# Kernel tuning notes

Measured on AMD Instinct MI355X. Metric: run time of the kernel, lower is better.

The kernel has to match this reference:

```python
import jax, jax.numpy as jnp
import numpy as np

N = 512
K = 32


def _laplacian_coo(n):
    """5-point stencil Laplacian on an n x n grid, COO (row, col, val)."""
    idx = np.arange(n * n).reshape(n, n)
    rows = [idx.ravel()]
    cols = [idx.ravel()]
    vals = [np.full(n * n, 4.0, dtype=np.float32)]
    # horizontal neighbors
    r = idx[:, 1:].ravel(); c = idx[:, :-1].ravel()
    rows += [r, c]; cols += [c, r]
    vals += [np.full(r.size, -1.0, dtype=np.float32)] * 2
    # vertical neighbors
    r = idx[1:, :].ravel(); c = idx[:-1, :].ravel()
    rows += [r, c]; cols += [c, r]
    vals += [np.full(r.size, -1.0, dtype=np.float32)] * 2
    return (np.concatenate(rows).astype(np.int32),
            np.concatenate(cols).astype(np.int32),
            np.concatenate(vals))


def setup_inputs() -> dict:
    key = jax.random.key(0)
    k_w, k_z = jax.random.split(key)
    # probe tensor with zeroed boundary (as in forward)
    w = jax.random.normal(k_w, (K, 1, N + 2, N + 2), dtype=jnp.float32)
    w = w.at[:, :, 0, :].set(0.0)
    w = w.at[:, :, -1, :].set(0.0)
    w = w.at[:, :, :, 0].set(0.0)
    w = w.at[:, :, :, -1].set(0.0)
    # stand-in for model(w): the network output flattened to (K, N*N)
    z = jax.random.normal(k_z, (K, N * N), dtype=jnp.float32)
    row, col, vals = _laplacian_coo(N)
    return {
        "w": w,
        "z": z,
        "row": jnp.asarray(row),
        "col": jnp.asarray(col),
        "vals": jnp.asarray(vals),
    }


def reference(w, z, row, col, vals):
    n2 = z.shape[1]                      # N*N
    # SpMM: Az = (A @ z^T)^T, done via gather + segment-sum over rows.
    gathered = vals[:, None] * z[:, col].T          # [nnz, K]
    Az = jax.ops.segment_sum(gathered, row, num_segments=n2).T  # [K, N*N]
    n = w.shape[-1] - 2
    w_interior = w[:, 0, 1:-1, 1:-1].reshape(w.shape[0], n * n)
    diff = w_interior - Az
    loss = jnp.mean(jnp.sum(diff * diff, axis=1))
    return loss
```

## Files before the change

### kernel.cpp

```cpp
#include <hip/hip_runtime.h>
#include <hip/hip_bf16.h>


#define N_GRID 512
#define K_PROBE 32
#define NN (N_GRID * N_GRID)
#define WROW (N_GRID + 2)
#define R_BAND 8
#define BANDS (N_GRID / R_BAND)
#define NBLOCKS ((K_PROBE * BANDS) / 2)

__global__ __launch_bounds__(256) void condition_loss_main(
    const float* __restrict__ w, const float* __restrict__ z,
    float* __restrict__ partial) {
    const int work = (blockIdx.x & 7) * (NBLOCKS / 8) + (blockIdx.x >> 3);

    const int band_g = work * 2 + (threadIdx.x >> 7);
    const int k    = band_g >> 6;
    const int band = band_g & 63;
    const int cg   = threadIdx.x & 127;
    const int col  = cg << 2;
    const int r0   = band * R_BAND;

    const float* __restrict__ zk = z + (long)k * NN + col;
    const float* __restrict__ wk =
        w + (long)k * (WROW * WROW) + (long)(r0 + 1) * WROW + (col + 1);

    float4 zm = make_float4(0.f, 0.f, 0.f, 0.f);
    if (r0 > 0) zm = *reinterpret_cast<const float4*>(zk + (long)(r0 - 1) * N_GRID);
    float4 zc = *reinterpret_cast<const float4*>(zk + (long)r0 * N_GRID);

    float acc = 0.0f;
#pragma unroll
    for (int r = 0; r < R_BAND; ++r) {
        const int i = r0 + r;
        float4 zp = make_float4(0.f, 0.f, 0.f, 0.f);
        if (i + 1 < N_GRID)
            zp = *reinterpret_cast<const float4*>(zk + (long)(i + 1) * N_GRID);
        const float zl = (col > 0)            ? zk[(long)i * N_GRID - 1] : 0.0f;
        const float zr = (col + 4 < N_GRID)   ? zk[(long)i * N_GRID + 4] : 0.0f;

        const float az0 = 4.0f * zc.x - zm.x - zp.x - zl   - zc.y;
        const float az1 = 4.0f * zc.y - zm.y - zp.y - zc.x - zc.z;
        const float az2 = 4.0f * zc.z - zm.z - zp.z - zc.y - zc.w;
        const float az3 = 4.0f * zc.w - zm.w - zp.w - zc.z - zr;

        const float* __restrict__ wr = wk + (long)r * WROW;
        const float d0 = wr[0] - az0;
        const float d1 = wr[1] - az1;
        const float d2 = wr[2] - az2;
        const float d3 = wr[3] - az3;
        acc += d0 * d0 + d1 * d1 + d2 * d2 + d3 * d3;

        zm = zc;
        zc = zp;
    }

    for (int off = 32; off > 0; off >>= 1) acc += __shfl_down(acc, off, 64);

    __shared__ float ssum[4];
    const int lane = threadIdx.x & 63;
    const int wid  = threadIdx.x >> 6;
    if (lane == 0) ssum[wid] = acc;
    __syncthreads();
    if (threadIdx.x == 0)
        partial[blockIdx.x] = ssum[0] + ssum[1] + ssum[2] + ssum[3];
}

__global__ __launch_bounds__(256) void condition_loss_finalize(
    const float* __restrict__ partial, float* __restrict__ out) {
    float acc = 0.0f;
    for (int i = threadIdx.x; i < NBLOCKS; i += 256) acc += partial[i];
    for (int off = 32; off > 0; off >>= 1) acc += __shfl_down(acc, off, 64);
    __shared__ float ssum[4];
    const int lane = threadIdx.x & 63;
    const int wid  = threadIdx.x >> 6;
    if (lane == 0) ssum[wid] = acc;
    __syncthreads();
    if (threadIdx.x == 0)
        out[0] = (ssum[0] + ssum[1] + ssum[2] + ssum[3]) * (1.0f / (float)K_PROBE);
}

extern "C" void kernel_launch(void* const* d_in, const int* in_sizes, int n_in,
                              void* d_out, int out_size, void* d_ws, size_t ws_size,
                              hipStream_t stream) {
    const float* w = (const float*)d_in[0];
    const float* z = (const float*)d_in[1];
    float* out     = (float*)d_out;
    float* partial = (float*)d_ws;

    condition_loss_main<<<NBLOCKS, 256, 0, stream>>>(w, z, partial);
    condition_loss_finalize<<<1, 256, 0, stream>>>(partial, out);
}
```

Measured before the change: 21.25 us.

## Use 2 columns per thread with shuffle-based horizontal neighbors

Each thread now handles 2 columns instead of 4, so a block covers one band of one probe and the grid doubles. Left and right neighbor values come from wavefront shuffles instead of extra scalar global loads, with only the edge lanes of each wavefront loading from memory. Launch bounds now request 8 blocks per SM to raise occupancy. The trade-off is narrower float2 loads, more threads and shuffle instructions, and more partial sums for the finalize kernel to reduce.

Result: slower. 22.06 us (+3.8%).

```diff
diff --git a/kernel.cpp b/kernel.cpp
--- a/kernel.cpp
+++ b/kernel.cpp
@@ -8,49 +8,46 @@
 #define WROW (N_GRID + 2)
 #define R_BAND 8
 #define BANDS (N_GRID / R_BAND)
-#define NBLOCKS ((K_PROBE * BANDS) / 2)
+#define NBLOCKS (K_PROBE * BANDS)
 
-__global__ __launch_bounds__(256) void condition_loss_main(
+__global__ __launch_bounds__(256, 8) void condition_loss_main(
     const float* __restrict__ w, const float* __restrict__ z,
     float* __restrict__ partial) {
-    const int work = (blockIdx.x & 7) * (NBLOCKS / 8) + (blockIdx.x >> 3);
-
-    const int band_g = work * 2 + (threadIdx.x >> 7);
-    const int k    = band_g >> 6;
-    const int band = band_g & 63;
-    const int cg   = threadIdx.x & 127;
-    const int col  = cg << 2;
+    const int blk  = (blockIdx.x & 7) * (NBLOCKS / 8) + (blockIdx.x >> 3);
+    const int k    = blk >> 6;
+    const int band = blk & (BANDS - 1);
     const int r0   = band * R_BAND;
+    const int col  = (int)(threadIdx.x << 1);
+    const int lane = threadIdx.x & 63;
 
     const float* __restrict__ zk = z + (long)k * NN + col;
     const float* __restrict__ wk =
         w + (long)k * (WROW * WROW) + (long)(r0 + 1) * WROW + (col + 1);
 
-    float4 zm = make_float4(0.f, 0.f, 0.f, 0.f);
-    if (r0 > 0) zm = *reinterpret_cast<const float4*>(zk + (long)(r0 - 1) * N_GRID);
-    float4 zc = *reinterpret_cast<const float4*>(zk + (long)r0 * N_GRID);
+    float2 zm = make_float2(0.f, 0.f);
+    if (r0 > 0) zm = *reinterpret_cast<const float2*>(zk + (long)(r0 - 1) * N_GRID);
+    float2 zc = *reinterpret_cast<const float2*>(zk + (long)r0 * N_GRID);
 
     float acc = 0.0f;
 #pragma unroll
     for (int r = 0; r < R_BAND; ++r) {
         const int i = r0 + r;
-        float4 zp = make_float4(0.f, 0.f, 0.f, 0.f);
+        float2 zp = make_float2(0.f, 0.f);
         if (i + 1 < N_GRID)
-            zp = *reinterpret_cast<const float4*>(zk + (long)(i + 1) * N_GRID);
-        const float zl = (col > 0)            ? zk[(long)i * N_GRID - 1] : 0.0f;
-        const float zr = (col + 4 < N_GRID)   ? zk[(long)i * N_GRID + 4] : 0.0f;
+            zp = *reinterpret_cast<const float2*>(zk + (long)(i + 1) * N_GRID);
+
+        float zl = __shfl_up(zc.y, 1, 64);
+        float zr = __shfl_down(zc.x, 1, 64);
+        if (lane == 0)  zl = (col > 0)            ? zk[(long)i * N_GRID - 1] : 0.0f;
+        if (lane == 63) zr = (col + 2 < N_GRID)   ? zk[(long)i * N_GRID + 2] : 0.0f;
 
         const float az0 = 4.0f * zc.x - zm.x - zp.x - zl   - zc.y;
-        const float az1 = 4.0f * zc.y - zm.y - zp.y - zc.x - zc.z;
-        const float az2 = 4.0f * zc.z - zm.z - zp.z - zc.y - zc.w;
-        const float az3 = 4.0f * zc.w - zm.w - zp.w - zc.z - zr;
+        const float az1 = 4.0f * zc.y - zm.y - zp.y - zc.x - zr;
 
         const float* __restrict__ wr = wk + (long)r * WROW;
         const float d0 = wr[0] - az0;
         const float d1 = wr[1] - az1;
-        const float d2 = wr[2] - az2;
-        const float d3 = wr[3] - az3;
-        acc += d0 * d0 + d1 * d1 + d2 * d2 + d3 * d3;
+        acc += d0 * d0 + d1 * d1;
 
         zm = zc;
         zc = zp;
@@ -59,8 +56,7 @@
     for (int off = 32; off > 0; off >>= 1) acc += __shfl_down(acc, off, 64);
 
     __shared__ float ssum[4];
-    const int lane = threadIdx.x & 63;
-    const int wid  = threadIdx.x >> 6;
+    const int wid = threadIdx.x >> 6;
     if (lane == 0) ssum[wid] = acc;
     __syncthreads();
     if (threadIdx.x == 0)
```
